# Performance work log

Hardware: AMD Instinct MI355X
Metric: run time of the kernel (lower is better)

## Reference

```python
import jax, jax.numpy as jnp
import numpy as np
import math

B, S, D, H = 2, 2048, 1024, 16
DK = D // H


def setup_inputs() -> dict:
    key = jax.random.key(0)
    ks = jax.random.split(key, 8)
    s = 1.0 / math.sqrt(D)
    inp = {
        "query": jax.random.normal(ks[0], (B, S, D), jnp.float32),
        "key": jax.random.normal(ks[1], (B, S, D), jnp.float32),
        "value": jax.random.normal(ks[2], (B, S, D), jnp.float32),
        # causal mask: (1, 1, S, S), 1 where attention allowed
        "mask": jnp.tril(jnp.ones((S, S), jnp.int32))[None, None, :, :],
        "Wq": jax.random.normal(ks[3], (D, D), jnp.float32) * s,
        "Wk": jax.random.normal(ks[4], (D, D), jnp.float32) * s,
        "Wv": jax.random.normal(ks[5], (D, D), jnp.float32) * s,
        "Wo": jax.random.normal(ks[6], (D, D), jnp.float32) * s,
    }
    return inp


def reference(query, key, value, mask, Wq, Wk, Wv, Wo):
    # nn.Linear(bias=False): y = x @ W.T
    def proj_heads(x, W):
        y = jnp.einsum("bsd,ed->bse", x, W)          # (B,S,D)
        return y.reshape(B, -1, H, DK).transpose(0, 2, 1, 3)  # (B,H,S,DK)

    q = proj_heads(query, Wq)
    k = proj_heads(key, Wk)
    v = proj_heads(value, Wv)

    scale = jnp.asarray(math.sqrt(DK), q.dtype)
    scores = jnp.einsum("bhqd,bhkd->bhqk", q, k) / scale  # (B,H,S,S)
    scores = jnp.where(mask == 0, -jnp.inf, scores)
    attn = jax.nn.softmax(scores, axis=-1)
    # dropout p=0.0 (eval): identity
    out = jnp.einsum("bhqk,bhkd->bhqd", attn, v)          # (B,H,S,DK)
    concat = out.transpose(0, 2, 1, 3).reshape(B, -1, D)  # (B,S,D)
    return jnp.einsum("bsd,ed->bse", concat, Wo)
```

## Files before the change

### kernel.cpp

```cpp
#include <hip/hip_runtime.h>
#include <hip/hip_bf16.h>

#define B_ 2
#define S_ 2048
#define D_ 1024
#define H_ 16
#define DK_ 64

typedef __hip_bfloat16 bf16;
typedef __attribute__((ext_vector_type(8))) short bf16x8;
typedef __attribute__((ext_vector_type(4))) short bf16x4;
typedef __attribute__((ext_vector_type(4))) float f32x4;

#define GLDS16(g, l)                                                     \
    __builtin_amdgcn_global_load_lds(                                    \
        (const __attribute__((address_space(1))) void*)(g),              \
        (__attribute__((address_space(3))) void*)(l), 16, 0, 0)

#define MFMA_K32(a, b, c) __builtin_amdgcn_mfma_f32_16x16x32_bf16(a, b, c, 0, 0, 0)
#define MFMA_K16(a, b, c) __builtin_amdgcn_mfma_f32_16x16x16bf16_1k(a, b, c, 0, 0, 0)
#define EXP2F(x) __builtin_amdgcn_exp2f(x)

__global__ __launch_bounds__(256) void cvt_all(
    const float* __restrict__ q, const float* __restrict__ k, const float* __restrict__ v,
    const float* __restrict__ w0, const float* __restrict__ w1,
    const float* __restrict__ w2, const float* __restrict__ w3,
    bf16* __restrict__ oq, bf16* __restrict__ ok, bf16* __restrict__ ov,
    bf16* __restrict__ o0, bf16* __restrict__ o1, bf16* __restrict__ o2,
    bf16* __restrict__ o3) {
    int bid = blockIdx.x;
    const float* src; bf16* dst; int base;
    if      (bid < 2048) { src = q;  dst = oq; base = bid; }
    else if (bid < 4096) { src = k;  dst = ok; base = bid - 2048; }
    else if (bid < 6144) { src = v;  dst = ov; base = bid - 4096; }
    else if (bid < 6656) { src = w0; dst = o0; base = bid - 6144; }
    else if (bid < 7168) { src = w1; dst = o1; base = bid - 6656; }
    else if (bid < 7680) { src = w2; dst = o2; base = bid - 7168; }
    else                 { src = w3; dst = o3; base = bid - 7680; }
    int i = (base * 256 + threadIdx.x) * 8;
    float4 a = *(const float4*)(src + i);
    float4 b = *(const float4*)(src + i + 4);
    __align__(16) bf16 o[8];
    o[0] = __float2bfloat16(a.x); o[1] = __float2bfloat16(a.y);
    o[2] = __float2bfloat16(a.z); o[3] = __float2bfloat16(a.w);
    o[4] = __float2bfloat16(b.x); o[5] = __float2bfloat16(b.y);
    o[6] = __float2bfloat16(b.z); o[7] = __float2bfloat16(b.w);
    *(bf16x8*)(dst + i) = *(const bf16x8*)o;
}

__device__ __forceinline__ void proj_loop64(const bf16* __restrict__ X,
                                            const bf16* __restrict__ W,
                                            int m0, int n0, bf16* As, bf16* Bs,
                                            f32x4 (&acc)[2][4]) {
    const int K = D_;
    const int tid = threadIdx.x;
    const int lane = tid & 63, wave = tid >> 6;
    const int lm = lane & 15, quad = lane >> 4;

    auto stage = [&](int t, int bf) {
        int k0 = t * 64;
        bf16* Ab = As + bf * (128 * 64);
        bf16* Bb = Bs + bf * (64 * 64);
#pragma unroll
        for (int i = 0; i < 4; ++i) {
            int s = i * 256 + tid;
            int row = s >> 3, c = (s & 7) ^ (row & 7);
            GLDS16(X + (size_t)(m0 + row) * K + k0 + c * 8, Ab + s * 8);
        }
#pragma unroll
        for (int i = 0; i < 2; ++i) {
            int s = i * 256 + tid;
            int row = s >> 3, c = (s & 7) ^ (row & 7);
            GLDS16(W + (size_t)(n0 + row) * K + k0 + c * 8, Bb + s * 8);
        }
    };

    stage(0, 0);
    for (int t = 0; t < K / 64; ++t) {
        __syncthreads();
        if (t + 1 < K / 64) stage(t + 1, (t + 1) & 1);
        const bf16* Ab = As + (t & 1) * (128 * 64);
        const bf16* Bb = Bs + (t & 1) * (64 * 64);
#pragma unroll
        for (int ks = 0; ks < 2; ++ks) {
            bf16x8 aF[2], bF[4];
#pragma unroll
            for (int mt = 0; mt < 2; ++mt) {
                int row = wave * 32 + mt * 16 + lm;
                aF[mt] = *(const bf16x8*)(Ab + row * 64 +
                                          ((ks * 4 + quad) ^ (row & 7)) * 8);
            }
#pragma unroll
            for (int nt = 0; nt < 4; ++nt) {
                int row = nt * 16 + lm;
                bF[nt] = *(const bf16x8*)(Bb + row * 64 +
                                          ((ks * 4 + quad) ^ (row & 7)) * 8);
            }
#pragma unroll
            for (int mt = 0; mt < 2; ++mt)
#pragma unroll
                for (int nt = 0; nt < 4; ++nt)
                    acc[mt][nt] = MFMA_K32(aF[mt], bF[nt], acc[mt][nt]);
        }
    }
}

__global__ __launch_bounds__(256) void proj_qkv(
    const bf16* __restrict__ qx, const bf16* __restrict__ kx, const bf16* __restrict__ vx,
    const bf16* __restrict__ wq, const bf16* __restrict__ wk, const bf16* __restrict__ wv,
    bf16* __restrict__ qb, bf16* __restrict__ kb, bf16* __restrict__ vtb) {
    __shared__ __align__(16) bf16 As[2 * 128 * 64];
    __shared__ __align__(16) bf16 Bs[2 * 64 * 64];
    const int z = blockIdx.z;
    const bf16* X = (z == 0) ? qx : (z == 1) ? kx : vx;
    const bf16* W = (z == 0) ? wq : (z == 1) ? wk : wv;
    const int n0 = blockIdx.x * 64;
    const int m0 = blockIdx.y * 128;
    f32x4 acc[2][4] = {};
    proj_loop64(X, W, m0, n0, As, Bs, acc);

    const int lane = threadIdx.x & 63, wave = threadIdx.x >> 6;
    const int lm = lane & 15, quad = lane >> 4;
#pragma unroll
    for (int mt = 0; mt < 2; ++mt) {
        int mbase = m0 + wave * 32 + mt * 16 + quad * 4;
#pragma unroll
        for (int nt = 0; nt < 4; ++nt) {
            int n = n0 + nt * 16 + lm;
            if (z == 2) {
                int b = mbase >> 11, s = mbase & (S_ - 1);
                unsigned short u[4];
#pragma unroll
                for (int r = 0; r < 4; ++r) {
                    bf16 hv = __float2bfloat16(acc[mt][nt][r]);
                    u[r] = *(unsigned short*)&hv;
                }
                ushort4 pk = {u[0], u[1], u[2], u[3]};
                *(ushort4*)(vtb + ((size_t)(b * 1024 + n) * S_ + s)) = pk;
            } else {
                bf16* Y = z ? kb : qb;
#pragma unroll
                for (int r = 0; r < 4; ++r)
                    Y[(size_t)(mbase + r) * D_ + n] = __float2bfloat16(acc[mt][nt][r]);
            }
        }
    }
}

__global__ __launch_bounds__(256) void proj_o(const bf16* __restrict__ X,
                                              const bf16* __restrict__ W,
                                              float* __restrict__ Y) {
    __shared__ __align__(16) bf16 As[2 * 128 * 64];
    __shared__ __align__(16) bf16 Bs[2 * 64 * 64];
    const int n0 = blockIdx.x * 64;
    const int m0 = blockIdx.y * 128;
    f32x4 acc[2][4] = {};
    proj_loop64(X, W, m0, n0, As, Bs, acc);

    const int lane = threadIdx.x & 63, wave = threadIdx.x >> 6;
    const int lm = lane & 15, quad = lane >> 4;
#pragma unroll
    for (int mt = 0; mt < 2; ++mt) {
        int mbase = m0 + wave * 32 + mt * 16 + quad * 4;
#pragma unroll
        for (int nt = 0; nt < 4; ++nt) {
            int n = n0 + nt * 16 + lm;
#pragma unroll
            for (int r = 0; r < 4; ++r)
                Y[(size_t)(mbase + r) * D_ + n] = acc[mt][nt][r];
        }
    }
}

__global__ __launch_bounds__(512) void attn_kernel(const bf16* __restrict__ Q,
                                                   const bf16* __restrict__ Kb,
                                                   const bf16* __restrict__ VT,
                                                   bf16* __restrict__ O) {
    __shared__ __align__(16) bf16 kt[2][128 * 64];
    __shared__ __align__(16) bf16 vt[2][64 * 128];

    const int tid = threadIdx.x;
    const int lane = tid & 63, wave = tid >> 6;
    const int lm = lane & 15, quad = lane >> 4;
    const int f = (int)blockIdx.x;
    const int cls = f & 7;
    const int t = f >> 3;
    const int qi = 15 - (t >> 2);
    const int combo = cls + 8 * (t & 3);
    const int b = combo >> 4, h = combo & 15;
    const int q0 = qi * 128 + wave * 16;

    const size_t bhoff = (size_t)b * S_ * D_ + (size_t)h * DK_;
    const bf16* vtb = VT + ((size_t)b * 1024 + h * DK_) * S_;

    const bf16* qp = Q + bhoff + (size_t)(q0 + lm) * D_ + quad * 8;
    bf16x8 aq0 = *(const bf16x8*)(qp);
    bf16x8 aq1 = *(const bf16x8*)(qp + 32);

    f32x4 oacc[4] = {};
    float lsum = 0.f;
    const float cexp = 0.125f * 1.44269504f;

    auto stage = [&](int i, int bf) {
        int j0s = i * 128;
#pragma unroll
        for (int ii = 0; ii < 2; ++ii) {
            int s = ii * 512 + tid;
            int j = s >> 3, c = (s & 7) ^ (j & 7);
            GLDS16(Kb + bhoff + (size_t)(j0s + j) * D_ + c * 8, kt[bf] + s * 8);
        }
#pragma unroll
        for (int ii = 0; ii < 2; ++ii) {
            int s = ii * 512 + tid;
            int d = s >> 4, c = (s & 15) ^ (d & 15);
            GLDS16(vtb + (size_t)d * S_ + j0s + c * 8, vt[bf] + s * 8);
        }
    };

    auto chunk = [&](const bf16* ktb, const bf16* vtl, int st, bool mk) {
        int j = st * 16 + lm;
        bf16x8 bk0 = *(const bf16x8*)(ktb + (((j << 3) | (quad ^ (j & 7))) * 8));
        bf16x8 bk1 = *(const bf16x8*)(ktb + (((j << 3) | ((4 + quad) ^ (j & 7))) * 8));
        f32x4 z = {};
        z = MFMA_K32(bk0, aq0, z);
        z = MFMA_K32(bk1, aq1, z);
        bf16x4 pa;
        float rs = 0.f;
#pragma unroll
        for (int r = 0; r < 4; ++r) {
            float p = EXP2F(z[r] * cexp);
            if (mk && (quad * 4 + r > lm)) p = 0.f;
            rs += p;
            bf16 hv = __float2bfloat16(p);
            pa[r] = *(short*)&hv;
        }
        lsum += rs;
#pragma unroll
        for (int dt = 0; dt < 4; ++dt) {
            int d = dt * 16 + lm;
            int cl = st * 2 + (quad >> 1);
            bf16x4 bv = *(const bf16x4*)(vtl + d * 128 +
                                         ((cl ^ (d & 15)) * 8 + (quad & 1) * 4));
            oacc[dt] = MFMA_K16(pa, bv, oacc[dt]);
        }
    };

    stage(0, 0);

    for (int i = 0; i <= qi; ++i) {
        __syncthreads();
        if (i < qi) stage(i + 1, (i + 1) & 1);
        const bf16* ktb = kt[i & 1];
        const bf16* vtl = vt[i & 1];
        if (i < qi) {
#pragma unroll
            for (int st = 0; st < 8; ++st) chunk(ktb, vtl, st, false);
        } else {
            for (int st = 0; st < wave; ++st) chunk(ktb, vtl, st, false);
            chunk(ktb, vtl, wave, true);
        }
    }

    float l = lsum;
    l += __shfl_xor(l, 16, 64);
    l += __shfl_xor(l, 32, 64);
#pragma unroll
    for (int r = 0; r < 4; ++r) {
        float inv = 1.f / __shfl(l, quad * 4 + r, 64);
        int qrow = q0 + quad * 4 + r;
#pragma unroll
        for (int dt = 0; dt < 4; ++dt) {
            int d = dt * 16 + lm;
            O[bhoff + (size_t)qrow * D_ + d] = __float2bfloat16(oacc[dt][r] * inv);
        }
    }
}

extern "C" void kernel_launch(void* const* d_in, const int* in_sizes, int n_in,
                              void* d_out, int out_size, void* d_ws, size_t ws_size,
                              hipStream_t stream) {
    const float* q_in = (const float*)d_in[0];
    const float* k_in = (const float*)d_in[1];
    const float* v_in = (const float*)d_in[2];
    const float* Wq_f = (const float*)d_in[4];
    const float* Wk_f = (const float*)d_in[5];
    const float* Wv_f = (const float*)d_in[6];
    const float* Wo_f = (const float*)d_in[7];
    float* out = (float*)d_out;

    const size_t NEL = (size_t)B_ * S_ * D_;
    const size_t WEL = (size_t)D_ * D_;
    bf16* p = (bf16*)d_ws;
    bf16* qx = p;  p += NEL;
    bf16* kx = p;  p += NEL;
    bf16* vx = p;  p += NEL;
    bf16* wq = p;  p += WEL;
    bf16* wk = p;  p += WEL;
    bf16* wv = p;  p += WEL;
    bf16* wo = p;  p += WEL;
    bf16* qb = p;  p += NEL;
    bf16* kb = p;  p += NEL;
    bf16* vtb = p; p += NEL;
    bf16* cb = p;  p += NEL;

    cvt_all<<<8192, 256, 0, stream>>>(q_in, k_in, v_in, Wq_f, Wk_f, Wv_f, Wo_f,
                                      qx, kx, vx, wq, wk, wv, wo);

    dim3 gqkv(D_ / 64, (B_ * S_) / 128, 3);
    proj_qkv<<<gqkv, 256, 0, stream>>>(qx, kx, vx, wq, wk, wv, qb, kb, vtb);

    attn_kernel<<<dim3(512), 512, 0, stream>>>(qb, kb, vtb, cb);

    dim3 gproj(D_ / 64, (B_ * S_) / 128);
    proj_o<<<gproj, 256, 0, stream>>>(cb, wo, out);
}
```

Baseline: 217.9 us.

## Widen projection GEMM tiles to 128x128 and remap blocks for XCD locality

New measurement: 232.4 us. 6.6% more time.

```diff
diff --git a/kernel.cpp b/kernel.cpp
--- a/kernel.cpp
+++ b/kernel.cpp
@@ -48,10 +48,10 @@
     *(bf16x8*)(dst + i) = *(const bf16x8*)o;
 }
 
-__device__ __forceinline__ void proj_loop64(const bf16* __restrict__ X,
-                                            const bf16* __restrict__ W,
-                                            int m0, int n0, bf16* As, bf16* Bs,
-                                            f32x4 (&acc)[2][4]) {
+__device__ __forceinline__ void proj_loop128(const bf16* __restrict__ X,
+                                             const bf16* __restrict__ W,
+                                             int m0, int n0, bf16* As, bf16* Bs,
+                                             f32x4 (&acc)[2][8]) {
     const int K = D_;
     const int tid = threadIdx.x;
     const int lane = tid & 63, wave = tid >> 6;
@@ -60,7 +60,7 @@
     auto stage = [&](int t, int bf) {
         int k0 = t * 64;
         bf16* Ab = As + bf * (128 * 64);
-        bf16* Bb = Bs + bf * (64 * 64);
+        bf16* Bb = Bs + bf * (128 * 64);
 #pragma unroll
         for (int i = 0; i < 4; ++i) {
             int s = i * 256 + tid;
@@ -68,7 +68,7 @@
             GLDS16(X + (size_t)(m0 + row) * K + k0 + c * 8, Ab + s * 8);
         }
 #pragma unroll
-        for (int i = 0; i < 2; ++i) {
+        for (int i = 0; i < 4; ++i) {
             int s = i * 256 + tid;
             int row = s >> 3, c = (s & 7) ^ (row & 7);
             GLDS16(W + (size_t)(n0 + row) * K + k0 + c * 8, Bb + s * 8);
@@ -80,10 +80,10 @@
         __syncthreads();
         if (t + 1 < K / 64) stage(t + 1, (t + 1) & 1);
         const bf16* Ab = As + (t & 1) * (128 * 64);
-        const bf16* Bb = Bs + (t & 1) * (64 * 64);
+        const bf16* Bb = Bs + (t & 1) * (128 * 64);
 #pragma unroll
         for (int ks = 0; ks < 2; ++ks) {
-            bf16x8 aF[2], bF[4];
+            bf16x8 aF[2], bF[8];
 #pragma unroll
             for (int mt = 0; mt < 2; ++mt) {
                 int row = wave * 32 + mt * 16 + lm;
@@ -91,7 +91,7 @@
                                           ((ks * 4 + quad) ^ (row & 7)) * 8);
             }
 #pragma unroll
-            for (int nt = 0; nt < 4; ++nt) {
+            for (int nt = 0; nt < 8; ++nt) {
                 int row = nt * 16 + lm;
                 bF[nt] = *(const bf16x8*)(Bb + row * 64 +
                                           ((ks * 4 + quad) ^ (row & 7)) * 8);
@@ -99,7 +99,7 @@
 #pragma unroll
             for (int mt = 0; mt < 2; ++mt)
 #pragma unroll
-                for (int nt = 0; nt < 4; ++nt)
+                for (int nt = 0; nt < 8; ++nt)
                     acc[mt][nt] = MFMA_K32(aF[mt], bF[nt], acc[mt][nt]);
         }
     }
@@ -110,14 +110,18 @@
     const bf16* __restrict__ wq, const bf16* __restrict__ wk, const bf16* __restrict__ wv,
     bf16* __restrict__ qb, bf16* __restrict__ kb, bf16* __restrict__ vtb) {
     __shared__ __align__(16) bf16 As[2 * 128 * 64];
-    __shared__ __align__(16) bf16 Bs[2 * 64 * 64];
-    const int z = blockIdx.z;
+    __shared__ __align__(16) bf16 Bs[2 * 128 * 64];
+    const int f = (int)blockIdx.x;
+    const int cls = f & 7, idx = f >> 3;
+    const int g = idx >> 3, n = idx & 7;
+    const int zm = cls + 8 * g;
+    const int z = zm >> 5, mi = zm & 31;
+    const int m0 = mi * 128, n0 = n * 128;
+
     const bf16* X = (z == 0) ? qx : (z == 1) ? kx : vx;
     const bf16* W = (z == 0) ? wq : (z == 1) ? wk : wv;
-    const int n0 = blockIdx.x * 64;
-    const int m0 = blockIdx.y * 128;
-    f32x4 acc[2][4] = {};
-    proj_loop64(X, W, m0, n0, As, Bs, acc);
+    f32x4 acc[2][8] = {};
+    proj_loop128(X, W, m0, n0, As, Bs, acc);
 
     const int lane = threadIdx.x & 63, wave = threadIdx.x >> 6;
     const int lm = lane & 15, quad = lane >> 4;
@@ -125,8 +129,8 @@
     for (int mt = 0; mt < 2; ++mt) {
         int mbase = m0 + wave * 32 + mt * 16 + quad * 4;
 #pragma unroll
-        for (int nt = 0; nt < 4; ++nt) {
-            int n = n0 + nt * 16 + lm;
+        for (int nt = 0; nt < 8; ++nt) {
+            int nn = n0 + nt * 16 + lm;
             if (z == 2) {
                 int b = mbase >> 11, s = mbase & (S_ - 1);
                 unsigned short u[4];
@@ -136,12 +140,12 @@
                     u[r] = *(unsigned short*)&hv;
                 }
                 ushort4 pk = {u[0], u[1], u[2], u[3]};
-                *(ushort4*)(vtb + ((size_t)(b * 1024 + n) * S_ + s)) = pk;
+                *(ushort4*)(vtb + ((size_t)(b * 1024 + nn) * S_ + s)) = pk;
             } else {
                 bf16* Y = z ? kb : qb;
 #pragma unroll
                 for (int r = 0; r < 4; ++r)
-                    Y[(size_t)(mbase + r) * D_ + n] = __float2bfloat16(acc[mt][nt][r]);
+                    Y[(size_t)(mbase + r) * D_ + nn] = __float2bfloat16(acc[mt][nt][r]);
             }
         }
     }
@@ -151,11 +155,14 @@
                                               const bf16* __restrict__ W,
                                               float* __restrict__ Y) {
     __shared__ __align__(16) bf16 As[2 * 128 * 64];
-    __shared__ __align__(16) bf16 Bs[2 * 64 * 64];
-    const int n0 = blockIdx.x * 64;
-    const int m0 = blockIdx.y * 128;
-    f32x4 acc[2][4] = {};
-    proj_loop64(X, W, m0, n0, As, Bs, acc);
+    __shared__ __align__(16) bf16 Bs[2 * 128 * 64];
+    const int f = (int)blockIdx.x;
+    const int cls = f & 7, idx = f >> 3;
+    const int g = idx >> 3, n = idx & 7;
+    const int mi = cls + 8 * g;
+    const int m0 = mi * 128, n0 = n * 128;
+    f32x4 acc[2][8] = {};
+    proj_loop128(X, W, m0, n0, As, Bs, acc);
 
     const int lane = threadIdx.x & 63, wave = threadIdx.x >> 6;
     const int lm = lane & 15, quad = lane >> 4;
@@ -163,11 +170,11 @@
     for (int mt = 0; mt < 2; ++mt) {
         int mbase = m0 + wave * 32 + mt * 16 + quad * 4;
 #pragma unroll
-        for (int nt = 0; nt < 4; ++nt) {
-            int n = n0 + nt * 16 + lm;
+        for (int nt = 0; nt < 8; ++nt) {
+            int nn = n0 + nt * 16 + lm;
 #pragma unroll
             for (int r = 0; r < 4; ++r)
-                Y[(size_t)(mbase + r) * D_ + n] = acc[mt][nt][r];
+                Y[(size_t)(mbase + r) * D_ + nn] = acc[mt][nt][r];
         }
     }
 }
@@ -306,11 +313,9 @@
     cvt_all<<<8192, 256, 0, stream>>>(q_in, k_in, v_in, Wq_f, Wk_f, Wv_f, Wo_f,
                                       qx, kx, vx, wq, wk, wv, wo);
 
-    dim3 gqkv(D_ / 64, (B_ * S_) / 128, 3);
-    proj_qkv<<<gqkv, 256, 0, stream>>>(qx, kx, vx, wq, wk, wv, qb, kb, vtb);
+    proj_qkv<<<dim3(768), 256, 0, stream>>>(qx, kx, vx, wq, wk, wv, qb, kb, vtb);
 
     attn_kernel<<<dim3(512), 512, 0, stream>>>(qb, kb, vtb, cb);
 
-    dim3 gproj(D_ / 64, (B_ * S_) / 128);
-    proj_o<<<gproj, 256, 0, stream>>>(cb, wo, out);
-}
+    proj_o<<<dim3(256), 256, 0, stream>>>(cb, wo, out);
+}
```
